# Kernel tuning notes

Measured on AMD Instinct MI355X. Metric: run time of the kernel, lower is better.

## Reference

```python
import jax, jax.numpy as jnp
import numpy as np

ZMAX = 92          # max atomic number in NLH table
BOHR = 0.52917721  # Bohr radius in Angstrom (au.BOHR)
ENERGY_UNIT = 1.0  # multiplier for 'Ha'
N_ATOMS = 100_000
N_EDGES = 6_400_000
TAB = (ZMAX + 1) ** 2  # 8649


def setup_inputs() -> dict:
    key = jax.random.key(0)
    k1, k2, k3, k4, k5, k6, k7 = jax.random.split(key, 7)
    species = jax.random.randint(k1, (N_ATOMS,), 0, 93, dtype=jnp.int32)
    edge_src = jax.random.randint(k2, (N_EDGES,), 0, N_ATOMS, dtype=jnp.int32)
    edge_dst = jax.random.randint(k3, (N_EDGES,), 0, N_ATOMS, dtype=jnp.int32)
    # distances kept away from zero (division by rijs)
    distances = 0.5 + 4.5 * jax.random.uniform(k4, (N_EDGES,), dtype=jnp.float32)
    switch = jax.random.uniform(k5, (N_EDGES,), dtype=jnp.float32)
    CS = jax.random.uniform(k6, (TAB, 3), dtype=jnp.float32)
    ALPHAS = jax.random.uniform(k7, (TAB, 3), dtype=jnp.float32) + 0.5
    return {"species": species, "edge_src": edge_src, "edge_dst": edge_dst,
            "distances": distances, "switch": switch, "CS": CS, "ALPHAS": ALPHAS}


def reference(species, edge_src, edge_dst, distances, switch, CS, ALPHAS):
    # pair index into (zmax+1)^2 coefficient table
    s12 = species[edge_src] + ZMAX * species[edge_dst]
    cs = CS[s12]          # [E, 3]
    alphas = ALPHAS[s12]  # [E, 3]
    Z = jnp.where(species > 0, species.astype(distances.dtype), 0.0)
    # 3-term exponential screening function
    phi = jnp.sum(cs * jnp.exp(-alphas * distances[:, None]), axis=-1)  # [E]
    ereppair = Z[edge_src] * Z[edge_dst] * phi * switch / distances
    erep_atomic = ENERGY_UNIT * 0.5 * BOHR * jax.ops.segment_sum(
        ereppair, edge_src, num_segments=species.shape[0])
    return erep_atomic
```

## Files before the change

### kernel.cpp

```cpp
#include <hip/hip_runtime.h>
#include <hip/hip_fp16.h>


#define ZMAX_C 92
#define TAB93  93
#define NTAB   (TAB93 * TAB93)
#define HALF_BOHR 0.264588605f
#define NBMAX 64
#define APB 2048
#define APB_LOG 11
#define SPLITS 16
#define TPB 256
#define EPT 16
#define BLK_EDGES (TPB * EPT)

typedef int            ivec4 __attribute__((ext_vector_type(4)));
typedef float          fvec4 __attribute__((ext_vector_type(4)));

#if __has_builtin(__builtin_amdgcn_rcpf)
#define FAST_RCP(x) __builtin_amdgcn_rcpf(x)
#else
#define FAST_RCP(x) (1.0f / (x))
#endif

__global__ __launch_bounds__(TPB) void p0_prep(
    const float* __restrict__ CS, const float* __restrict__ ALPHAS,
    const int* __restrict__ species,
    uint4* __restrict__ tab16, unsigned char* __restrict__ spc8,
    unsigned* __restrict__ cursor, int n_atoms, int nb)
{
    int i = blockIdx.x * TPB + threadIdx.x;
    if (i < NTAB) {
        int sd = i / TAB93;
        int ss = i - TAB93 * sd;
        int ref = ss + ZMAX_C * sd;
        float Z = (ss > 0 && sd > 0) ? (float)(ss * sd) : 0.0f;
        __half h[8];
        h[0] = __float2half_rn(CS[3*ref+0] * Z);
        h[1] = __float2half_rn(CS[3*ref+1] * Z);
        h[2] = __float2half_rn(CS[3*ref+2] * Z);
        h[3] = __float2half_rn(-ALPHAS[3*ref+0]);
        h[4] = __float2half_rn(-ALPHAS[3*ref+1]);
        h[5] = __float2half_rn(-ALPHAS[3*ref+2]);
        h[6] = __half(0.0f); h[7] = __half(0.0f);
        tab16[i] = *reinterpret_cast<uint4*>(h);
    }
    if (i < n_atoms) spc8[i] = (unsigned char)species[i];
    if (i < nb) cursor[i] = 0u;
}

__device__ __forceinline__ float half_lo(unsigned u) {
    return __half2float(*reinterpret_cast<const __half*>(&u));
}
__device__ __forceinline__ float half_hi(unsigned u) {
    unsigned s = u >> 16;
    return __half2float(*reinterpret_cast<const __half*>(&s));
}

__global__ __launch_bounds__(TPB) void p1_bin(
    const int* __restrict__ edge_src, const int* __restrict__ edge_dst,
    const float* __restrict__ dist, const float* __restrict__ swt,
    const unsigned char* __restrict__ spc8, const uint4* __restrict__ tab16,
    unsigned* __restrict__ pairs, unsigned* __restrict__ cursor,
    int nb, int cap, int n_edges)
{
    __shared__ unsigned stage[BLK_EDGES];
    __shared__ unsigned hist[NBMAX];
    __shared__ unsigned lbase[NBMAX];
    __shared__ unsigned gbase[NBMAX];

    int tid = threadIdx.x;
    if (tid < NBMAX) hist[tid] = 0;
    __syncthreads();

    int lane = tid & 63, wave = tid >> 6;
    long long wbase = (long long)blockIdx.x * BLK_EDGES + (long long)wave * (64 * EPT);

    unsigned meta[EPT];
    unsigned short s12r[EPT];

    for (int jj = 0; jj < EPT / 8; ++jj) {
        long long eA = wbase + (jj*2+0) * 256 + lane * 4;
        long long eB = wbase + (jj*2+1) * 256 + lane * 4;
        int srcA[4], dstA[4], srcB[4], dstB[4];
        bool fullB = (eB + 3 < (long long)n_edges);
        if (fullB) {
            ivec4 s4 = __builtin_nontemporal_load((const ivec4*)(edge_src + eA));
            ivec4 d4 = __builtin_nontemporal_load((const ivec4*)(edge_dst + eA));
            ivec4 s5 = __builtin_nontemporal_load((const ivec4*)(edge_src + eB));
            ivec4 d5 = __builtin_nontemporal_load((const ivec4*)(edge_dst + eB));
            #pragma unroll
            for (int k = 0; k < 4; ++k) {
                srcA[k] = s4[k]; dstA[k] = d4[k];
                srcB[k] = s5[k]; dstB[k] = d5[k];
            }
        } else {
            #pragma unroll
            for (int k = 0; k < 4; ++k) {
                long long ea = eA + k, eb = eB + k;
                bool va = (ea < (long long)n_edges), vb = (eb < (long long)n_edges);
                srcA[k] = va ? edge_src[ea] : 0;  dstA[k] = va ? edge_dst[ea] : 0;
                srcB[k] = vb ? edge_src[eb] : 0;  dstB[k] = vb ? edge_dst[eb] : 0;
            }
        }
        int ssA[4], sdA[4], ssB[4], sdB[4];
        #pragma unroll
        for (int k = 0; k < 4; ++k) { ssA[k] = spc8[srcA[k]]; sdA[k] = spc8[dstA[k]]; }
        #pragma unroll
        for (int k = 0; k < 4; ++k) { ssB[k] = spc8[srcB[k]]; sdB[k] = spc8[dstB[k]]; }
        #pragma unroll
        for (int g = 0; g < 2; ++g) {
            const int* src = g ? srcB : srcA;
            const int* ss  = g ? ssB  : ssA;
            const int* sd  = g ? sdB  : sdA;
            long long  e0  = g ? eB   : eA;
            #pragma unroll
            for (int k = 0; k < 4; ++k) {
                int idx = jj * 8 + g * 4 + k;
                s12r[idx] = (unsigned short)(ss[k] + TAB93 * sd[k]);
                meta[idx] = 0u;
                if (e0 + k < (long long)n_edges) {
                    unsigned b    = (unsigned)src[k] >> APB_LOG;
                    unsigned lsrc = (unsigned)src[k] & (APB - 1);
                    unsigned rank = atomicAdd(&hist[b], 1u);
                    meta[idx] = 0x80000000u | (rank << 17) | (b << 11) | lsrc;
                }
            }
        }
    }
    __syncthreads();
    if (tid < 64) {
        unsigned v = (tid < nb) ? hist[tid] : 0u;
        unsigned x = v;
        #pragma unroll
        for (int off = 1; off < 64; off <<= 1) {
            unsigned y = __shfl_up(x, off);
            if ((tid & 63) >= off) x += y;
        }
        if (tid < nb) lbase[tid] = x - v;
    }
    __syncthreads();
    if (tid < nb) {
        unsigned c = hist[tid];
        gbase[tid] = c ? atomicAdd(cursor + tid, c) : 0u;
    }
    __syncthreads();

    for (int jj = 0; jj < EPT / 8; ++jj) {
        long long eA = wbase + (jj*2+0) * 256 + lane * 4;
        long long eB = wbase + (jj*2+1) * 256 + lane * 4;
        float rA[4], wA[4], rB[4], wB[4];
        bool fullB = (eB + 3 < (long long)n_edges);
        if (fullB) {
            fvec4 r4 = __builtin_nontemporal_load((const fvec4*)(dist + eA));
            fvec4 w4 = __builtin_nontemporal_load((const fvec4*)(swt + eA));
            fvec4 r5 = __builtin_nontemporal_load((const fvec4*)(dist + eB));
            fvec4 w5 = __builtin_nontemporal_load((const fvec4*)(swt + eB));
            #pragma unroll
            for (int k = 0; k < 4; ++k) {
                rA[k] = r4[k]; wA[k] = w4[k]; rB[k] = r5[k]; wB[k] = w5[k];
            }
        } else {
            #pragma unroll
            for (int k = 0; k < 4; ++k) {
                long long ea = eA + k, eb = eB + k;
                bool va = (ea < (long long)n_edges), vb = (eb < (long long)n_edges);
                rA[k] = va ? dist[ea] : 1.f;  wA[k] = va ? swt[ea] : 0.f;
                rB[k] = vb ? dist[eb] : 1.f;  wB[k] = vb ? swt[eb] : 0.f;
            }
        }
        uint4 tA[4], tB[4];
        #pragma unroll
        for (int k = 0; k < 4; ++k) tA[k] = tab16[s12r[jj*8 + k]];
        #pragma unroll
        for (int k = 0; k < 4; ++k) tB[k] = tab16[s12r[jj*8 + 4 + k]];
        #pragma unroll
        for (int g = 0; g < 2; ++g) {
            const float* r = g ? rB : rA;
            const float* w = g ? wB : wA;
            const uint4* t = g ? tB : tA;
            #pragma unroll
            for (int k = 0; k < 4; ++k) {
                int idx = jj * 8 + g * 4 + k;
                unsigned m = meta[idx];
                if (!(m & 0x80000000u)) continue;
                float c0 = half_lo(t[k].x), c1 = half_hi(t[k].x);
                float c2 = half_lo(t[k].y), na0 = half_hi(t[k].y);
                float na1 = half_lo(t[k].z), na2 = half_hi(t[k].z);
                float phi = c0 * __expf(na0 * r[k])
                          + c1 * __expf(na1 * r[k])
                          + c2 * __expf(na2 * r[k]);
                float val = HALF_BOHR * phi * w[k] * FAST_RCP(r[k]);
                unsigned pos = lbase[(m >> 11) & 63u] + ((m >> 17) & 0x3FFFu);
                unsigned short hb = __half_as_ushort(__float2half_rn(val));
                stage[pos] = ((m & (APB - 1)) << 16) | (unsigned)hb;
            }
        }
    }
    __syncthreads();
    for (int b = wave; b < nb; b += 4) {
        unsigned cnt = hist[b], lb = lbase[b], gb = gbase[b];
        unsigned* dst = pairs + (size_t)b * (size_t)cap + gb;
        for (unsigned i = lane; i < cnt; i += 64)
            if (gb + i < (unsigned)cap) dst[i] = stage[lb + i];
    }
}

__global__ __launch_bounds__(TPB) void p2a_reduce(
    const unsigned* __restrict__ pairs, const unsigned* __restrict__ cursor,
    float* __restrict__ partial, int cap, int stride)
{
    int b = blockIdx.x / SPLITS;
    int s = blockIdx.x % SPLITS;
    __shared__ float acc[APB];
    for (int i = threadIdx.x; i < APB; i += TPB) acc[i] = 0.f;
    __syncthreads();
    unsigned cnt = cursor[b];
    if (cnt > (unsigned)cap) cnt = (unsigned)cap;
    unsigned beg = (unsigned)((unsigned long long)cnt * s / SPLITS);
    unsigned end = (unsigned)((unsigned long long)cnt * (s + 1) / SPLITS);
    const unsigned* p = pairs + (size_t)b * (size_t)cap;
    unsigned i = beg + threadIdx.x;
    for (; i + 7u * TPB < end; i += 8u * TPB) {
        unsigned v[8];
        #pragma unroll
        for (int k = 0; k < 8; ++k) v[k] = p[i + (unsigned)k * TPB];
        #pragma unroll
        for (int k = 0; k < 8; ++k)
            unsafeAtomicAdd(&acc[v[k] >> 16],
                __half2float(__ushort_as_half((unsigned short)(v[k] & 0xFFFFu))));
    }
    for (; i < end; i += TPB) {
        unsigned v = p[i];
        unsafeAtomicAdd(&acc[v >> 16],
            __half2float(__ushort_as_half((unsigned short)(v & 0xFFFFu))));
    }
    __syncthreads();
    float* prow = partial + (size_t)s * stride + (size_t)b * APB;
    for (int k = threadIdx.x; k < APB; k += TPB) prow[k] = acc[k];
}

__global__ __launch_bounds__(TPB) void p2b_sum(
    const float* __restrict__ partial, float* __restrict__ out, int n, int stride)
{
    int i = blockIdx.x * TPB + threadIdx.x;
    if (i >= n) return;
    float s = 0.f;
    #pragma unroll
    for (int x = 0; x < SPLITS; ++x) s += partial[(size_t)x * stride + i];
    out[i] = s;
}

__global__ __launch_bounds__(TPB) void erep_edges_direct(
    const int* __restrict__ edge_src, const int* __restrict__ edge_dst,
    const float* __restrict__ dist, const float* __restrict__ swt,
    const int* __restrict__ species, const float* __restrict__ CS,
    const float* __restrict__ ALPHAS, float* __restrict__ out, int n_edges)
{
    int e = blockIdx.x * TPB + threadIdx.x;
    if (e >= n_edges) return;
    int ss = species[edge_src[e]], sd = species[edge_dst[e]];
    int prod = ss * sd;
    if (prod == 0) return;
    int s12 = ss + ZMAX_C * sd;
    float r = dist[e];
    float phi = CS[3*s12+0] * __expf(-ALPHAS[3*s12+0] * r)
              + CS[3*s12+1] * __expf(-ALPHAS[3*s12+1] * r)
              + CS[3*s12+2] * __expf(-ALPHAS[3*s12+2] * r);
    atomicAdd(out + edge_src[e],
              HALF_BOHR * (float)prod * phi * swt[e] * FAST_RCP(r));
}

extern "C" void kernel_launch(void* const* d_in, const int* in_sizes, int n_in,
                              void* d_out, int out_size, void* d_ws, size_t ws_size,
                              hipStream_t stream)
{
    const int*   species  = (const int*)  d_in[0];
    const int*   edge_src = (const int*)  d_in[1];
    const int*   edge_dst = (const int*)  d_in[2];
    const float* dist     = (const float*)d_in[3];
    const float* swt      = (const float*)d_in[4];
    const float* CS       = (const float*)d_in[5];
    const float* ALPHAS   = (const float*)d_in[6];
    float* out = (float*)d_out;

    int n_atoms = in_sizes[0];
    int n_edges = in_sizes[1];

    int nb = (n_atoms + APB - 1) / APB;
    long long capll = (long long)n_edges / nb + (long long)n_edges / ((long long)nb * 32) + 256;
    int cap = (int)((capll + 31) & ~31LL);
    int stride = nb * APB;

    size_t pairs_sz = ((size_t)nb * (size_t)cap * 4 + 255) & ~(size_t)255;
    size_t cur_sz   = ((size_t)nb * 4 + 255) & ~(size_t)255;
    size_t part_sz  = ((size_t)SPLITS * (size_t)stride * 4 + 255) & ~(size_t)255;
    size_t tab_sz   = ((size_t)NTAB * 16 + 255) & ~(size_t)255;
    size_t spc_sz   = ((size_t)n_atoms + 255) & ~(size_t)255;
    size_t need = pairs_sz + cur_sz + part_sz + tab_sz + spc_sz;

    if (nb <= NBMAX && n_edges > 0 && ws_size >= need) {
        char* w = (char*)d_ws;
        unsigned*       pairs   = (unsigned*)w;
        unsigned*       cursor  = (unsigned*)(w + pairs_sz);
        float*          partial = (float*)(w + pairs_sz + cur_sz);
        uint4*          tab16   = (uint4*)(w + pairs_sz + cur_sz + part_sz);
        unsigned char*  spc8    = (unsigned char*)(w + pairs_sz + cur_sz + part_sz + tab_sz);

        int pmax = n_atoms > NTAB ? n_atoms : NTAB;
        p0_prep<<<(pmax + TPB - 1) / TPB, TPB, 0, stream>>>(
            CS, ALPHAS, species, tab16, spc8, cursor, n_atoms, nb);

        p1_bin<<<(n_edges + BLK_EDGES - 1) / BLK_EDGES, TPB, 0, stream>>>(
            edge_src, edge_dst, dist, swt, spc8, tab16,
            pairs, cursor, nb, cap, n_edges);

        p2a_reduce<<<nb * SPLITS, TPB, 0, stream>>>(pairs, cursor, partial, cap, stride);
        p2b_sum<<<(n_atoms + TPB - 1) / TPB, TPB, 0, stream>>>(partial, out, n_atoms, stride);
    } else {
        (void)hipMemsetAsync(d_out, 0, (size_t)out_size * sizeof(float), stream);
        erep_edges_direct<<<(n_edges + TPB - 1) / TPB, TPB, 0, stream>>>(
            edge_src, edge_dst, dist, swt, species, CS, ALPHAS, out, n_edges);
    }
}
```

Before: 249.7 us.

## Use per-wave LDS histograms, batch all gathers, and vectorize reduce loads

The binning kernel now keeps one shared-memory histogram per wave, which cuts LDS atomic contention. Per-wave offsets are folded in with a small prefix step, and the global cursor atomics merge into the scan thread. All 16 edge index loads and species gathers are issued together before binning to raise memory-level parallelism, at some cost in registers. The reduce kernel reads packed pairs as uint4 vectors with tail masking, which assumes 16-byte alignment of each bin's row (cap a multiple of 4).

```diff
diff --git a/kernel.cpp b/kernel.cpp
--- a/kernel.cpp
+++ b/kernel.cpp
@@ -65,12 +65,16 @@
     int nb, int cap, int n_edges)
 {
     __shared__ unsigned stage[BLK_EDGES];
+    __shared__ unsigned hist4[4][NBMAX];
     __shared__ unsigned hist[NBMAX];
     __shared__ unsigned lbase[NBMAX];
     __shared__ unsigned gbase[NBMAX];
 
     int tid = threadIdx.x;
-    if (tid < NBMAX) hist[tid] = 0;
+    if (tid < NBMAX) {
+        hist4[0][tid] = 0; hist4[1][tid] = 0;
+        hist4[2][tid] = 0; hist4[3][tid] = 0;
+    }
     __syncthreads();
 
     int lane = tid & 63, wave = tid >> 6;
@@ -79,50 +83,43 @@
     unsigned meta[EPT];
     unsigned short s12r[EPT];
 
-    for (int jj = 0; jj < EPT / 8; ++jj) {
-        long long eA = wbase + (jj*2+0) * 256 + lane * 4;
-        long long eB = wbase + (jj*2+1) * 256 + lane * 4;
-        int srcA[4], dstA[4], srcB[4], dstB[4];
-        bool fullB = (eB + 3 < (long long)n_edges);
-        if (fullB) {
-            ivec4 s4 = __builtin_nontemporal_load((const ivec4*)(edge_src + eA));
-            ivec4 d4 = __builtin_nontemporal_load((const ivec4*)(edge_dst + eA));
-            ivec4 s5 = __builtin_nontemporal_load((const ivec4*)(edge_src + eB));
-            ivec4 d5 = __builtin_nontemporal_load((const ivec4*)(edge_dst + eB));
+    {
+        int srcv[EPT], dstv[EPT];
+        #pragma unroll
+        for (int j = 0; j < EPT / 4; ++j) {
+            long long e0 = wbase + j * 256 + lane * 4;
+            if (e0 + 3 < (long long)n_edges) {
+                ivec4 s4 = __builtin_nontemporal_load((const ivec4*)(edge_src + e0));
+                ivec4 d4 = __builtin_nontemporal_load((const ivec4*)(edge_dst + e0));
+                #pragma unroll
+                for (int k = 0; k < 4; ++k) { srcv[j*4+k] = s4[k]; dstv[j*4+k] = d4[k]; }
+            } else {
+                #pragma unroll
+                for (int k = 0; k < 4; ++k) {
+                    long long e = e0 + k;
+                    bool v = (e < (long long)n_edges);
+                    srcv[j*4+k] = v ? edge_src[e] : 0;
+                    dstv[j*4+k] = v ? edge_dst[e] : 0;
+                }
+            }
+        }
+        int ssv[EPT], sdv[EPT];
+        #pragma unroll
+        for (int i = 0; i < EPT; ++i) ssv[i] = spc8[srcv[i]];
+        #pragma unroll
+        for (int i = 0; i < EPT; ++i) sdv[i] = spc8[dstv[i]];
+        #pragma unroll
+        for (int j = 0; j < EPT / 4; ++j) {
+            long long e0 = wbase + j * 256 + lane * 4;
             #pragma unroll
             for (int k = 0; k < 4; ++k) {
-                srcA[k] = s4[k]; dstA[k] = d4[k];
-                srcB[k] = s5[k]; dstB[k] = d5[k];
-            }
-        } else {
-            #pragma unroll
-            for (int k = 0; k < 4; ++k) {
-                long long ea = eA + k, eb = eB + k;
-                bool va = (ea < (long long)n_edges), vb = (eb < (long long)n_edges);
-                srcA[k] = va ? edge_src[ea] : 0;  dstA[k] = va ? edge_dst[ea] : 0;
-                srcB[k] = vb ? edge_src[eb] : 0;  dstB[k] = vb ? edge_dst[eb] : 0;
-            }
-        }
-        int ssA[4], sdA[4], ssB[4], sdB[4];
-        #pragma unroll
-        for (int k = 0; k < 4; ++k) { ssA[k] = spc8[srcA[k]]; sdA[k] = spc8[dstA[k]]; }
-        #pragma unroll
-        for (int k = 0; k < 4; ++k) { ssB[k] = spc8[srcB[k]]; sdB[k] = spc8[dstB[k]]; }
-        #pragma unroll
-        for (int g = 0; g < 2; ++g) {
-            const int* src = g ? srcB : srcA;
-            const int* ss  = g ? ssB  : ssA;
-            const int* sd  = g ? sdB  : sdA;
-            long long  e0  = g ? eB   : eA;
-            #pragma unroll
-            for (int k = 0; k < 4; ++k) {
-                int idx = jj * 8 + g * 4 + k;
-                s12r[idx] = (unsigned short)(ss[k] + TAB93 * sd[k]);
+                int idx = j * 4 + k;
+                s12r[idx] = (unsigned short)(ssv[idx] + TAB93 * sdv[idx]);
                 meta[idx] = 0u;
                 if (e0 + k < (long long)n_edges) {
-                    unsigned b    = (unsigned)src[k] >> APB_LOG;
-                    unsigned lsrc = (unsigned)src[k] & (APB - 1);
-                    unsigned rank = atomicAdd(&hist[b], 1u);
+                    unsigned b    = (unsigned)srcv[idx] >> APB_LOG;
+                    unsigned lsrc = (unsigned)srcv[idx] & (APB - 1);
+                    unsigned rank = atomicAdd(&hist4[wave][b], 1u);
                     meta[idx] = 0x80000000u | (rank << 17) | (b << 11) | lsrc;
                 }
             }
@@ -130,19 +127,25 @@
     }
     __syncthreads();
     if (tid < 64) {
-        unsigned v = (tid < nb) ? hist[tid] : 0u;
+        unsigned h0 = hist4[0][tid], h1 = hist4[1][tid];
+        unsigned h2 = hist4[2][tid], h3 = hist4[3][tid];
+        unsigned tot = h0 + h1 + h2 + h3;
+        hist4[0][tid] = 0;
+        hist4[1][tid] = h0;
+        hist4[2][tid] = h0 + h1;
+        hist4[3][tid] = h0 + h1 + h2;
+        if (tid < nb) hist[tid] = tot;
+        unsigned v = (tid < nb) ? tot : 0u;
         unsigned x = v;
         #pragma unroll
         for (int off = 1; off < 64; off <<= 1) {
             unsigned y = __shfl_up(x, off);
             if ((tid & 63) >= off) x += y;
         }
-        if (tid < nb) lbase[tid] = x - v;
-    }
-    __syncthreads();
-    if (tid < nb) {
-        unsigned c = hist[tid];
-        gbase[tid] = c ? atomicAdd(cursor + tid, c) : 0u;
+        if (tid < nb) {
+            lbase[tid] = x - v;
+            gbase[tid] = v ? atomicAdd(cursor + tid, v) : 0u;
+        }
     }
     __syncthreads();
 
@@ -191,7 +194,8 @@
                           + c1 * __expf(na1 * r[k])
                           + c2 * __expf(na2 * r[k]);
                 float val = HALF_BOHR * phi * w[k] * FAST_RCP(r[k]);
-                unsigned pos = lbase[(m >> 11) & 63u] + ((m >> 17) & 0x3FFFu);
+                unsigned b = (m >> 11) & 63u;
+                unsigned pos = lbase[b] + hist4[wave][b] + ((m >> 17) & 0x3FFFu);
                 unsigned short hb = __half_as_ushort(__float2half_rn(val));
                 stage[pos] = ((m & (APB - 1)) << 16) | (unsigned)hb;
             }
@@ -217,23 +221,26 @@
     __syncthreads();
     unsigned cnt = cursor[b];
     if (cnt > (unsigned)cap) cnt = (unsigned)cap;
-    unsigned beg = (unsigned)((unsigned long long)cnt * s / SPLITS);
-    unsigned end = (unsigned)((unsigned long long)cnt * (s + 1) / SPLITS);
-    const unsigned* p = pairs + (size_t)b * (size_t)cap;
-    unsigned i = beg + threadIdx.x;
-    for (; i + 7u * TPB < end; i += 8u * TPB) {
-        unsigned v[8];
-        #pragma unroll
-        for (int k = 0; k < 8; ++k) v[k] = p[i + (unsigned)k * TPB];
-        #pragma unroll
-        for (int k = 0; k < 8; ++k)
-            unsafeAtomicAdd(&acc[v[k] >> 16],
-                __half2float(__ushort_as_half((unsigned short)(v[k] & 0xFFFFu))));
-    }
-    for (; i < end; i += TPB) {
-        unsigned v = p[i];
-        unsafeAtomicAdd(&acc[v >> 16],
-            __half2float(__ushort_as_half((unsigned short)(v & 0xFFFFu))));
+    unsigned nq = (cnt + 3u) >> 2;
+    unsigned qb = (unsigned)((unsigned long long)nq * s / SPLITS);
+    unsigned qe = (unsigned)((unsigned long long)nq * (s + 1) / SPLITS);
+    const uint4* p4 = (const uint4*)(pairs + (size_t)b * (size_t)cap);
+    for (unsigned q = qb + threadIdx.x; q < qe; q += TPB) {
+        uint4 v = p4[q];
+        unsigned base = q << 2;
+        if (base + 3u < cnt) {
+            unsafeAtomicAdd(&acc[v.x >> 16], __half2float(__ushort_as_half((unsigned short)(v.x & 0xFFFFu))));
+            unsafeAtomicAdd(&acc[v.y >> 16], __half2float(__ushort_as_half((unsigned short)(v.y & 0xFFFFu))));
+            unsafeAtomicAdd(&acc[v.z >> 16], __half2float(__ushort_as_half((unsigned short)(v.z & 0xFFFFu))));
+            unsafeAtomicAdd(&acc[v.w >> 16], __half2float(__ushort_as_half((unsigned short)(v.w & 0xFFFFu))));
+        } else {
+            unsigned vv[4] = {v.x, v.y, v.z, v.w};
+            #pragma unroll
+            for (int e = 0; e < 4; ++e)
+                if (base + (unsigned)e < cnt)
+                    unsafeAtomicAdd(&acc[vv[e] >> 16],
+                        __half2float(__ushort_as_half((unsigned short)(vv[e] & 0xFFFFu))));
+        }
     }
     __syncthreads();
     float* prow = partial + (size_t)s * stride + (size_t)b * APB;
```

Measured after the change: 249.0 us. Within noise of the previous version (-0.3%).
